# Optimization experiments

Measured on AMD Instinct MI355X. Metric: run time of the kernel, lower is better.

The kernel has to match this reference:

```python
import jax, jax.numpy as jnp
import numpy as np

NUM_HEADS = 16

def setup_inputs() -> dict:
    key = jax.random.key(0)
    k0, k1, k2, k3 = jax.random.split(key, 4)
    B, N, Nl, Nr, D = 16, 257, 514, 512, 1024
    gather_idx = jax.random.randint(k0, (B, N), 0, B * Nl + Nr, dtype=jnp.int64 if jax.config.jax_enable_x64 else jnp.int32)
    lhs_states = jax.random.normal(k1, (4, B, Nl, D), dtype=jnp.float32)
    rhs_states = jax.random.normal(k2, (4, 1, Nr, D), dtype=jnp.float32)
    Wo = jax.random.normal(k3, (D, D), dtype=jnp.float32) * 0.02
    bo = jnp.zeros((D,), dtype=jnp.float32)
    return {"gather_idx": gather_idx, "lhs_states": lhs_states, "rhs_states": rhs_states, "Wo": Wo, "bo": bo}


def _gather_stacked_batched_states(gather_idx, lhs_states, rhs_states):
    # lhs_states: [4, B, Nl, D] cache; rhs_states: [4, 1, Nr, D]
    # torch builds batched_states [4, 1, B*Nl+Nr, D] then gathers with [4, B, N, D] idx
    S, B, Nl, D = lhs_states.shape
    Nr = rhs_states.shape[2]
    batched = jnp.concatenate(
        [lhs_states.reshape(S, B * Nl, D), rhs_states.reshape(S, Nr, D)], axis=1
    )  # [4, B*Nl+Nr, D]
    N = gather_idx.shape[1]
    gathered = jnp.take(batched, gather_idx.reshape(-1), axis=1)  # [4, B*N, D]
    return gathered.reshape(S, B, N, D)


def reference(gather_idx, lhs_states, rhs_states, Wo, bo):
    # Gather hidden/q/k/v states from the expanded cache buffer (token reuse dispatch)
    gathered = _gather_stacked_batched_states(gather_idx, lhs_states, rhs_states)
    hidden, q, k, v = gathered[0], gathered[1], gathered[2], gathered[3]
    B, N, D = hidden.shape
    H = NUM_HEADS
    hd = D // H
    scale = hd ** -0.5
    # _shape: [B, N, D] -> [B, H, N, hd]; query scaled before bmm as in torch
    qh = (q * scale).reshape(B, N, H, hd).transpose(0, 2, 1, 3)
    kh = k.reshape(B, N, H, hd).transpose(0, 2, 1, 3)
    vh = v.reshape(B, N, H, hd).transpose(0, 2, 1, 3)
    attn_weights = jax.nn.softmax(jnp.einsum('bhqd,bhkd->bhqk', qh, kh), axis=-1)
    attn_out = jnp.einsum('bhqk,bhkd->bhqd', attn_weights, vh)  # [B, H, N, hd]
    attn_out = attn_out.transpose(0, 2, 1, 3).reshape(B, N, D)
    attn_out = attn_out @ Wo.T + bo  # out_proj (torch Linear)
    return hidden + attn_out  # residual
```

## Files before the change

kernel.cpp:

```cpp
#include <hip/hip_runtime.h>
#include <hip/hip_bf16.h>

typedef __attribute__((ext_vector_type(8))) short bf16x8;
typedef __attribute__((ext_vector_type(4))) float f32x4;
typedef unsigned short u16;
typedef unsigned int u32;

#define LHS_STRIDE 8421376
#define RHS_STRIDE 524288
#define TBL_SPLIT  8224
#define AN 257
#define KSD 68
#define VSD 292
#define PSD 292
#define GSD 40

__device__ __forceinline__ const float* tbl_row(int s, int g,
    const float* __restrict__ lhs, const float* __restrict__ rhs) {
  if (g < TBL_SPLIT) return lhs + (size_t)s * LHS_STRIDE + (size_t)g * 1024;
  return rhs + (size_t)s * RHS_STRIDE + (size_t)(g - TBL_SPLIT) * 1024;
}

__device__ __forceinline__ u16 f2b(float x) {
  union { __hip_bfloat16 b; u16 u; } c;
  c.b = __float2bfloat16(x);
  return c.u;
}

__device__ __forceinline__ bf16x8 mk8(ushort4 a, ushort4 b) {
  bf16x8 r;
  r[0] = (short)a.x; r[1] = (short)a.y; r[2] = (short)a.z; r[3] = (short)a.w;
  r[4] = (short)b.x; r[5] = (short)b.y; r[6] = (short)b.z; r[7] = (short)b.w;
  return r;
}

struct __align__(16) AttnSmem {
  int idx[260];
  u16 K[272 * KSD];
  u16 VT[64 * VSD];
  u16 P[4 * 16 * PSD];
};

__global__ __launch_bounds__(256, 1) void attn_kernel(
    const int* __restrict__ gidx, const float* __restrict__ lhs,
    const float* __restrict__ rhs, u16* __restrict__ attn_out) {
  __shared__ AttnSmem sm;
  const int bh = blockIdx.x, b = bh >> 4, h = bh & 15;
  const int t = threadIdx.x, wave = t >> 6, lane = t & 63;
  const int lg = lane >> 4, lr = lane & 15;

  {
    u32* p = (u32*)sm.K;
    const int nw = (272 * KSD + 64 * VSD + 4 * 16 * PSD) / 2;
    for (int i = t; i < nw; i += 256) p[i] = 0u;
  }
  for (int i = t; i < AN; i += 256) sm.idx[i] = gidx[b * AN + i];
  __syncthreads();

  {
    const int sr = t >> 4, c4 = (t & 15) * 4;
    for (int pass = 0; pass < 17; ++pass) {
      int r = pass * 16 + sr;
      if (r < AN) {
        int g = sm.idx[r];
        float4 kv = *(const float4*)(tbl_row(2, g, lhs, rhs) + h * 64 + c4);
        *(ushort4*)&sm.K[r * KSD + c4] =
            make_ushort4(f2b(kv.x), f2b(kv.y), f2b(kv.z), f2b(kv.w));
        float4 vv = *(const float4*)(tbl_row(3, g, lhs, rhs) + h * 64 + c4);
        sm.VT[(c4 + 0) * VSD + r] = f2b(vv.x);
        sm.VT[(c4 + 1) * VSD + r] = f2b(vv.y);
        sm.VT[(c4 + 2) * VSD + r] = f2b(vv.z);
        sm.VT[(c4 + 3) * VSD + r] = f2b(vv.w);
      }
    }
  }
  __syncthreads();

  u16* Pw = sm.P + wave * 16 * PSD;
  for (int iter = 0; iter < 5; ++iter) {
    const int r0 = iter * 64 + wave * 16;

    bf16x8 qa[2];
    {
      int qrow = r0 + lr;
      int g = sm.idx[qrow < AN ? qrow : 0];
      const float* qp = tbl_row(1, g, lhs, rhs) + h * 64 + lg * 8;
#pragma unroll
      for (int kf = 0; kf < 2; ++kf) {
        float4 v0 = *(const float4*)(qp + kf * 32);
        float4 v1 = *(const float4*)(qp + kf * 32 + 4);
        bf16x8 a;
        a[0] = (short)f2b(0.125f * v0.x); a[1] = (short)f2b(0.125f * v0.y);
        a[2] = (short)f2b(0.125f * v0.z); a[3] = (short)f2b(0.125f * v0.w);
        a[4] = (short)f2b(0.125f * v1.x); a[5] = (short)f2b(0.125f * v1.y);
        a[6] = (short)f2b(0.125f * v1.z); a[7] = (short)f2b(0.125f * v1.w);
        qa[kf] = a;
      }
    }

    f32x4 s[17];
#pragma unroll
    for (int nf = 0; nf < 17; ++nf) {
      const u16* kp = &sm.K[(nf * 16 + lr) * KSD + lg * 8];
      ushort4 x0 = *(const ushort4*)kp;
      ushort4 x1 = *(const ushort4*)(kp + 4);
      ushort4 y0 = *(const ushort4*)(kp + 32);
      ushort4 y1 = *(const ushort4*)(kp + 36);
      f32x4 acc = {0.f, 0.f, 0.f, 0.f};
      acc = __builtin_amdgcn_mfma_f32_16x16x32_bf16(qa[0], mk8(x0, x1), acc, 0, 0, 0);
      acc = __builtin_amdgcn_mfma_f32_16x16x32_bf16(qa[1], mk8(y0, y1), acc, 0, 0, 0);
      s[nf] = acc;
    }
    if (lr != 0) { s[16][0] = -1e30f; s[16][1] = -1e30f; s[16][2] = -1e30f; s[16][3] = -1e30f; }

    float inv[4];
#pragma unroll
    for (int reg = 0; reg < 4; ++reg) {
      float m = -1e30f;
#pragma unroll
      for (int nf = 0; nf < 17; ++nf) m = fmaxf(m, s[nf][reg]);
#pragma unroll
      for (int off = 1; off < 16; off <<= 1) m = fmaxf(m, __shfl_xor(m, off, 16));
      float sum = 0.f;
#pragma unroll
      for (int nf = 0; nf < 17; ++nf) {
        float w = __expf(s[nf][reg] - m);
        s[nf][reg] = w;
        sum += w;
      }
#pragma unroll
      for (int off = 1; off < 16; off <<= 1) sum += __shfl_xor(sum, off, 16);
      inv[reg] = 1.0f / sum;
    }
#pragma unroll
    for (int reg = 0; reg < 4; ++reg) {
#pragma unroll
      for (int nf = 0; nf < 17; ++nf)
        Pw[(lg * 4 + reg) * PSD + nf * 16 + lr] = f2b(s[nf][reg] * inv[reg]);
    }

    f32x4 zero = {0.f, 0.f, 0.f, 0.f};
    f32x4 o[4] = {zero, zero, zero, zero};
#pragma unroll
    for (int ks = 0; ks < 9; ++ks) {
      const u16* pp = &Pw[lr * PSD + ks * 32 + lg * 8];
      bf16x8 pa = mk8(*(const ushort4*)pp, *(const ushort4*)(pp + 4));
#pragma unroll
      for (int nd = 0; nd < 4; ++nd) {
        const u16* vp = &sm.VT[(nd * 16 + lr) * VSD + ks * 32 + lg * 8];
        bf16x8 vb = mk8(*(const ushort4*)vp, *(const ushort4*)(vp + 4));
        o[nd] = __builtin_amdgcn_mfma_f32_16x16x32_bf16(pa, vb, o[nd], 0, 0, 0);
      }
    }

#pragma unroll
    for (int nd = 0; nd < 4; ++nd)
#pragma unroll
      for (int reg = 0; reg < 4; ++reg) {
        int row = r0 + lg * 4 + reg;
        if (row < AN)
          attn_out[(size_t)(b * AN + row) * 1024 + h * 64 + nd * 16 + lr] =
              f2b(o[nd][reg]);
      }
  }
}

__global__ void cvt_wo_kernel(const float* __restrict__ w, u16* __restrict__ o) {
  int i = blockIdx.x * 256 + threadIdx.x;
  float4 v = ((const float4*)w)[i];
  ((ushort4*)o)[i] = make_ushort4(f2b(v.x), f2b(v.y), f2b(v.z), f2b(v.w));
}

__global__ __launch_bounds__(256, 1) void gemm_kernel(
    const u16* __restrict__ A, const u16* __restrict__ Bw,
    const float* __restrict__ bo, const int* __restrict__ gidx,
    const float* __restrict__ lhs, const float* __restrict__ rhs,
    float* __restrict__ out) {
  __shared__ __align__(16) u16 As[128 * GSD];
  __shared__ __align__(16) u16 Bs[128 * GSD];
  const int t = threadIdx.x, wave = t >> 6, lane = t & 63;
  const int lg = lane >> 4, lr = lane & 15;
  const int mt = blockIdx.x >> 3, nt = blockIdx.x & 7;
  const int m0 = mt * 128, n0 = nt * 128;
  const int wm = wave >> 1, wn = wave & 1;

  f32x4 zero = {0.f, 0.f, 0.f, 0.f};
  f32x4 acc[4][4];
#pragma unroll
  for (int i = 0; i < 4; ++i)
#pragma unroll
    for (int j = 0; j < 4; ++j) acc[i][j] = zero;

  const int srow = t >> 2, scol = (t & 3) * 8;
  for (int kt = 0; kt < 32; ++kt) {
    const int k0 = kt * 32;
#pragma unroll
    for (int p = 0; p < 2; ++p) {
      int row = srow + p * 64;
      int gar = m0 + row; if (gar > 4111) gar = 4111;
      uint4 va = *(const uint4*)(A + (size_t)gar * 1024 + k0 + scol);
      *(uint4*)&As[row * GSD + scol] = va;
      uint4 vb = *(const uint4*)(Bw + (size_t)(n0 + row) * 1024 + k0 + scol);
      *(uint4*)&Bs[row * GSD + scol] = vb;
    }
    __syncthreads();
    bf16x8 af[4], bfr[4];
#pragma unroll
    for (int i = 0; i < 4; ++i) {
      af[i]  = *(const bf16x8*)&As[(wm * 64 + i * 16 + lr) * GSD + lg * 8];
      bfr[i] = *(const bf16x8*)&Bs[(wn * 64 + i * 16 + lr) * GSD + lg * 8];
    }
#pragma unroll
    for (int i = 0; i < 4; ++i)
#pragma unroll
      for (int j = 0; j < 4; ++j)
        acc[i][j] = __builtin_amdgcn_mfma_f32_16x16x32_bf16(af[i], bfr[j], acc[i][j], 0, 0, 0);
    __syncthreads();
  }

#pragma unroll
  for (int i = 0; i < 4; ++i)
#pragma unroll
    for (int j = 0; j < 4; ++j)
#pragma unroll
      for (int reg = 0; reg < 4; ++reg) {
        int row = m0 + wm * 64 + i * 16 + lg * 4 + reg;
        int col = n0 + wn * 64 + j * 16 + lr;
        if (row < 4112) {
          int g = gidx[row];
          out[(size_t)row * 1024 + col] =
              tbl_row(0, g, lhs, rhs)[col] + bo[col] + acc[i][j][reg];
        }
      }
}

extern "C" void kernel_launch(void* const* d_in, const int* in_sizes, int n_in,
                              void* d_out, int out_size, void* d_ws, size_t ws_size,
                              hipStream_t stream) {
  const int*   gidx = (const int*)d_in[0];
  const float* lhs  = (const float*)d_in[1];
  const float* rhs  = (const float*)d_in[2];
  const float* Wo   = (const float*)d_in[3];
  const float* bo   = (const float*)d_in[4];
  float* out = (float*)d_out;

  u16* attn_ws = (u16*)d_ws;
  u16* wo_bf   = attn_ws + (size_t)4112 * 1024;

  cvt_wo_kernel<<<1024, 256, 0, stream>>>(Wo, wo_bf);
  attn_kernel<<<256, 256, 0, stream>>>(gidx, lhs, rhs, attn_ws);
  gemm_kernel<<<264, 256, 0, stream>>>(attn_ws, wo_bf, bo, gidx, lhs, rhs, out);
}
```

Measured before the change: 283.7 us.

## Double attention waves per block and use direct global-to-LDS loads with swizzle in GEMM

The attention kernel now runs 512 threads (8 waves) per head. Each wave takes 16-row tiles in a strided loop, which shortens the per-block serial work and halves the K/V staging passes. The GEMM stops staging tiles through registers and uses global_load_lds 16-byte transfers into an unpadded LDS layout, with an XOR swizzle on the column chunk to avoid bank conflicts. Zeroing of the K buffer is dropped, so K padding rows are no longer cleared, and the swizzle has to match the wave-contiguous LDS write order that global_load_lds imposes.

Measured after the change: 262.9 us. 1.08x faster.

```diff
diff --git a/kernel.cpp b/kernel.cpp
--- a/kernel.cpp
+++ b/kernel.cpp
@@ -13,7 +13,6 @@
 #define KSD 68
 #define VSD 292
 #define PSD 292
-#define GSD 40
 
 __device__ __forceinline__ const float* tbl_row(int s, int g,
     const float* __restrict__ lhs, const float* __restrict__ rhs) {
@@ -34,14 +33,20 @@
   return r;
 }
 
+__device__ __forceinline__ void gload16(const u16* g, u16* l) {
+  __builtin_amdgcn_global_load_lds((const __attribute__((address_space(1))) void*)g,
+                                   (__attribute__((address_space(3))) void*)l,
+                                   16, 0, 0);
+}
+
 struct __align__(16) AttnSmem {
   int idx[260];
   u16 K[272 * KSD];
   u16 VT[64 * VSD];
-  u16 P[4 * 16 * PSD];
+  u16 P[8 * 16 * PSD];
 };
 
-__global__ __launch_bounds__(256, 1) void attn_kernel(
+__global__ __launch_bounds__(512, 1) void attn_kernel(
     const int* __restrict__ gidx, const float* __restrict__ lhs,
     const float* __restrict__ rhs, u16* __restrict__ attn_out) {
   __shared__ AttnSmem sm;
@@ -50,17 +55,18 @@
   const int lg = lane >> 4, lr = lane & 15;
 
   {
-    u32* p = (u32*)sm.K;
-    const int nw = (272 * KSD + 64 * VSD + 4 * 16 * PSD) / 2;
-    for (int i = t; i < nw; i += 256) p[i] = 0u;
-  }
-  for (int i = t; i < AN; i += 256) sm.idx[i] = gidx[b * AN + i];
+    uint4 z = {0u, 0u, 0u, 0u};
+    uint4* p = (uint4*)sm.VT;
+    const int n16 = (64 * VSD + 8 * 16 * PSD) * 2 / 16;
+    for (int i = t; i < n16; i += 512) p[i] = z;
+  }
+  for (int i = t; i < AN; i += 512) sm.idx[i] = gidx[b * AN + i];
   __syncthreads();
 
   {
     const int sr = t >> 4, c4 = (t & 15) * 4;
-    for (int pass = 0; pass < 17; ++pass) {
-      int r = pass * 16 + sr;
+    for (int pass = 0; pass < 9; ++pass) {
+      int r = pass * 32 + sr;
       if (r < AN) {
         int g = sm.idx[r];
         float4 kv = *(const float4*)(tbl_row(2, g, lhs, rhs) + h * 64 + c4);
@@ -77,8 +83,8 @@
   __syncthreads();
 
   u16* Pw = sm.P + wave * 16 * PSD;
-  for (int iter = 0; iter < 5; ++iter) {
-    const int r0 = iter * 64 + wave * 16;
+  for (int rt = wave; rt < 17; rt += 8) {
+    const int r0 = rt * 16;
 
     bf16x8 qa[2];
     {
@@ -176,8 +182,8 @@
     const float* __restrict__ bo, const int* __restrict__ gidx,
     const float* __restrict__ lhs, const float* __restrict__ rhs,
     float* __restrict__ out) {
-  __shared__ __align__(16) u16 As[128 * GSD];
-  __shared__ __align__(16) u16 Bs[128 * GSD];
+  __shared__ __align__(16) u16 As[128 * 32];
+  __shared__ __align__(16) u16 Bs[128 * 32];
   const int t = threadIdx.x, wave = t >> 6, lane = t & 63;
   const int lg = lane >> 4, lr = lane & 15;
   const int mt = blockIdx.x >> 3, nt = blockIdx.x & 7;
@@ -191,24 +197,25 @@
 #pragma unroll
     for (int j = 0; j < 4; ++j) acc[i][j] = zero;
 
-  const int srow = t >> 2, scol = (t & 3) * 8;
+  const int srow = lane >> 2;
+  const int scol = (((lane & 3) ^ ((lane >> 3) & 3))) * 8;
+  const int ss = (lg ^ ((lr >> 1) & 3)) * 8;
+
   for (int kt = 0; kt < 32; ++kt) {
     const int k0 = kt * 32;
 #pragma unroll
-    for (int p = 0; p < 2; ++p) {
-      int row = srow + p * 64;
-      int gar = m0 + row; if (gar > 4111) gar = 4111;
-      uint4 va = *(const uint4*)(A + (size_t)gar * 1024 + k0 + scol);
-      *(uint4*)&As[row * GSD + scol] = va;
-      uint4 vb = *(const uint4*)(Bw + (size_t)(n0 + row) * 1024 + k0 + scol);
-      *(uint4*)&Bs[row * GSD + scol] = vb;
+    for (int i = 0; i < 2; ++i) {
+      int row = wave * 32 + i * 16 + srow;
+      int arow = m0 + row; if (arow > 4111) arow = 4111;
+      gload16(A + (size_t)arow * 1024 + k0 + scol, &As[wave * 1024 + i * 512]);
+      gload16(Bw + (size_t)(n0 + row) * 1024 + k0 + scol, &Bs[wave * 1024 + i * 512]);
     }
     __syncthreads();
     bf16x8 af[4], bfr[4];
 #pragma unroll
     for (int i = 0; i < 4; ++i) {
-      af[i]  = *(const bf16x8*)&As[(wm * 64 + i * 16 + lr) * GSD + lg * 8];
-      bfr[i] = *(const bf16x8*)&Bs[(wn * 64 + i * 16 + lr) * GSD + lg * 8];
+      af[i]  = *(const bf16x8*)&As[(wm * 64 + i * 16 + lr) * 32 + ss];
+      bfr[i] = *(const bf16x8*)&Bs[(wn * 64 + i * 16 + lr) * 32 + ss];
     }
 #pragma unroll
     for (int i = 0; i < 4; ++i)
@@ -248,6 +255,6 @@
   u16* wo_bf   = attn_ws + (size_t)4112 * 1024;
 
   cvt_wo_kernel<<<1024, 256, 0, stream>>>(Wo, wo_bf);
-  attn_kernel<<<256, 256, 0, stream>>>(gidx, lhs, rhs, attn_ws);
+  attn_kernel<<<256, 512, 0, stream>>>(gidx, lhs, rhs, attn_ws);
   gemm_kernel<<<264, 256, 0, stream>>>(attn_ws, wo_bf, bo, gidx, lhs, rhs, out);
 }
```
